# Performance work log

Hardware: AMD Instinct MI355X
Metric: run time of the kernel (lower is better)

The kernel has to match this reference:

```python
import jax, jax.numpy as jnp
import numpy as np

B = 100000
MEM_DIM = 256
EDGE_DIM = 172
TIME_DIM = 100
NODE_DIM = 128
P = 5  # num_prototypes
LN_EPS = 1e-5
TEMP_MIN, TEMP_MAX = 0.05, 2.0


def _xavier(key, shape):
    fan_out, fan_in = shape
    lim = jnp.sqrt(6.0 / (fan_in + fan_out))
    return jax.random.uniform(key, shape, jnp.float32, -lim, lim)


def setup_inputs() -> dict:
    key = jax.random.key(0)
    ks = jax.random.split(key, 8)
    qin = MEM_DIM + EDGE_DIM + TIME_DIM
    gin = 2 * MEM_DIM + TIME_DIM
    return {
        "raw_memory": jax.random.normal(ks[0], (B, MEM_DIM), jnp.float32),
        "node_features": jax.random.normal(ks[1], (B, NODE_DIM), jnp.float32),
        "edge_features": jax.random.normal(ks[2], (B, EDGE_DIM), jnp.float32),
        "time_encoding": jax.random.normal(ks[3], (B, TIME_DIM), jnp.float32),
        "prototypes": jax.random.normal(ks[4], (B, P, MEM_DIM), jnp.float32),
        "Wq": _xavier(ks[5], (MEM_DIM, qin)),
        "bq": jnp.zeros((MEM_DIM,), jnp.float32),
        "Wg": _xavier(ks[6], (1, gin)),
        "bg": jnp.ones((1,), jnp.float32),
        "temperature": jnp.ones((1,), jnp.float32) * 0.1,
        "ln_gamma": jnp.ones((MEM_DIM,), jnp.float32),
        "ln_beta": jnp.zeros((MEM_DIM,), jnp.float32),
        "node_mask": jax.random.randint(ks[7], (B, P), 0, 2).astype(bool),
    }


def _layernorm(x, gamma, beta):
    mu = jnp.mean(x, axis=-1, keepdims=True)
    var = jnp.var(x, axis=-1, keepdims=True)
    return (x - mu) * jax.lax.rsqrt(var + LN_EPS) * gamma + beta


def _l2norm(x):
    n = jnp.sqrt(jnp.sum(x * x, axis=-1, keepdims=True))
    return x / jnp.maximum(n, 1e-12)


def reference(raw_memory, node_features, edge_features, time_encoding, prototypes,
              Wq, bq, Wg, bg, temperature, ln_gamma, ln_beta, node_mask):
    raw_memory = jnp.nan_to_num(raw_memory, nan=0.0, posinf=10.0, neginf=-10.0)
    edge_features = jnp.nan_to_num(edge_features, nan=0.0, posinf=10.0, neginf=-10.0)

    # fused query path: concat -> linear -> layernorm -> tanh
    query_inputs = jnp.concatenate([raw_memory, edge_features, time_encoding], axis=-1)
    query = query_inputs @ Wq.T + bq
    query = jnp.tanh(_layernorm(query, ln_gamma, ln_beta))  # [B, D]

    # cosine similarity against per-node prototypes [B, P, D]
    qn = _l2norm(query)
    pn = _l2norm(prototypes)
    sim = jnp.einsum('bd,bpd->bp', qn, pn)
    temp = jnp.clip(temperature, TEMP_MIN, TEMP_MAX)
    sim = sim / (temp + 1e-6)

    # masked softmax with uniform fallback for fully-masked rows
    sim = jnp.where(node_mask, sim, -jnp.inf)
    all_masked = jnp.all(~node_mask, axis=-1, keepdims=True)
    safe_sim = jnp.where(all_masked, jnp.zeros_like(sim), sim)
    attn = jax.nn.softmax(safe_sim, axis=-1)  # uniform where all masked

    cand = jnp.einsum('bp,bpd->bd', attn, prototypes)
    cand = jnp.clip(cand, -5.0, 5.0)

    gate_inputs = jnp.concatenate([raw_memory, cand, time_encoding], axis=-1)
    gate_inputs = jnp.clip(gate_inputs, -100.0, 100.0)
    gate = jax.nn.sigmoid(gate_inputs @ Wg.T + bg)  # [B, 1]

    updated = (1.0 - gate) * raw_memory + gate * cand
    updated = jnp.clip(_layernorm(updated, ln_gamma, ln_beta), -50.0, 50.0)
    return (updated, attn, gate, cand, query, sim)
```

## Files before the change

### kernel.cpp

```cpp
#include <hip/hip_runtime.h>
#include <math.h>

#define BB 100000
#define DM 256
#define EM 172
#define TM 100
#define QIN 528
#define NP 5

#define OFF_ATTN (256*BB)
#define OFF_GATE (261*BB)
#define OFF_CAND (262*BB)
#define OFF_QRY  (518*BB)
#define OFF_SIM  (774*BB)

__device__ __forceinline__ float ntn(float v) {
  if (v != v) return 0.0f;
  if (isinf(v)) return v > 0.0f ? 10.0f : -10.0f;
  return v;
}

__device__ __forceinline__ float clipf(float v, float lo, float hi) {
  return fminf(fmaxf(v, lo), hi);
}

#define BM 64
#define KC 16

__global__ __launch_bounds__(256)
void k_gemm(const float* __restrict__ raw, const float* __restrict__ edg,
            const float* __restrict__ tim, const float* __restrict__ Wq,
            const float* __restrict__ bq, float* __restrict__ qout)
{
  __shared__ float As[KC][BM];
  __shared__ float Ws[KC][DM];
  const int tid = threadIdx.x;
  const int ty = tid >> 5;
  const int tx = tid & 31;
  const int row0 = (int)blockIdx.x * BM;

  float acc[8][8];
#pragma unroll
  for (int i = 0; i < 8; ++i)
#pragma unroll
    for (int j = 0; j < 8; ++j) acc[i][j] = 0.0f;

  for (int k0 = 0; k0 < QIN; k0 += KC) {
#pragma unroll
    for (int j = 0; j < 4; ++j) {
      int e = tid * 4 + j;
      int r = e >> 4;
      int kk = e & 15;
      int row = row0 + r; row = row < BB ? row : BB - 1;
      int k = k0 + kk;
      float v;
      if (k < DM)           v = ntn(raw[row * DM + k]);
      else if (k < DM + EM) v = ntn(edg[row * EM + (k - DM)]);
      else                  v = tim[row * TM + (k - DM - EM)];
      As[kk][r] = v;
    }
    {
      const float* wr = Wq + tid * QIN + k0;
#pragma unroll
      for (int kk = 0; kk < KC; ++kk) Ws[kk][tid] = wr[kk];
    }
    __syncthreads();
#pragma unroll
    for (int kk = 0; kk < KC; ++kk) {
      float4 a0 = *(const float4*)&As[kk][ty * 8];
      float4 a1 = *(const float4*)&As[kk][ty * 8 + 4];
      float4 b0 = *(const float4*)&Ws[kk][tx * 8];
      float4 b1 = *(const float4*)&Ws[kk][tx * 8 + 4];
      float a[8] = {a0.x,a0.y,a0.z,a0.w,a1.x,a1.y,a1.z,a1.w};
      float b[8] = {b0.x,b0.y,b0.z,b0.w,b1.x,b1.y,b1.z,b1.w};
#pragma unroll
      for (int i = 0; i < 8; ++i)
#pragma unroll
        for (int j = 0; j < 8; ++j) acc[i][j] = fmaf(a[i], b[j], acc[i][j]);
    }
    __syncthreads();
  }

  const int c0 = tx * 8;
  float4 q0 = *(const float4*)&bq[c0];
  float4 q1 = *(const float4*)&bq[c0 + 4];
  float bqv[8] = {q0.x,q0.y,q0.z,q0.w,q1.x,q1.y,q1.z,q1.w};
#pragma unroll
  for (int i = 0; i < 8; ++i) {
    int row = row0 + ty * 8 + i;
    if (row < BB) {
      float4 o0 = make_float4(acc[i][0]+bqv[0], acc[i][1]+bqv[1],
                              acc[i][2]+bqv[2], acc[i][3]+bqv[3]);
      float4 o1 = make_float4(acc[i][4]+bqv[4], acc[i][5]+bqv[5],
                              acc[i][6]+bqv[6], acc[i][7]+bqv[7]);
      *(float4*)&qout[row * DM + c0]     = o0;
      *(float4*)&qout[row * DM + c0 + 4] = o1;
    }
  }
}

__global__ __launch_bounds__(256)
void k_epi(const float* __restrict__ raw, const float* __restrict__ tim,
           const float* __restrict__ pro, const float* __restrict__ Wg,
           const float* __restrict__ bg, const float* __restrict__ tpr,
           const float* __restrict__ gam, const float* __restrict__ bet,
           const unsigned char* __restrict__ msk, float* out)
{
  const int lane = threadIdx.x & 63;
  const int wid  = ((int)blockIdx.x * (int)blockDim.x + (int)threadIdx.x) >> 6;
  const int nw   = ((int)gridDim.x * (int)blockDim.x) >> 6;
  const int c0   = lane * 4;

  const float temp = fminf(fmaxf(tpr[0], 0.05f), 2.0f) + 1e-6f;
  const float bgv  = bg[0];
  const float4 gm4 = *(const float4*)&gam[c0];
  const float4 bt4 = *(const float4*)&bet[c0];
  const float ga[4] = {gm4.x, gm4.y, gm4.z, gm4.w};
  const float be[4] = {bt4.x, bt4.y, bt4.z, bt4.w};
  const float4 wr_ = *(const float4*)&Wg[c0];
  const float4 wc_ = *(const float4*)&Wg[DM + c0];
  float4 wt_ = make_float4(0.f, 0.f, 0.f, 0.f);
  if (lane < TM/4) wt_ = *(const float4*)&Wg[2*DM + c0];

  for (int row = wid; row < BB; row += nw) {
    const float4 qp = *(const float4*)&out[OFF_QRY + row*DM + c0];
    float s  = qp.x + qp.y + qp.z + qp.w;
    float ss = qp.x*qp.x + qp.y*qp.y + qp.z*qp.z + qp.w*qp.w;
#pragma unroll
    for (int m = 32; m; m >>= 1) { s += __shfl_xor(s, m); ss += __shfl_xor(ss, m); }
    const float mu   = s * (1.0f/DM);
    const float rstd = rsqrtf(ss*(1.0f/DM) - mu*mu + 1e-5f);
    float q[4];
    q[0] = tanhf((qp.x - mu)*rstd*ga[0] + be[0]);
    q[1] = tanhf((qp.y - mu)*rstd*ga[1] + be[1]);
    q[2] = tanhf((qp.z - mu)*rstd*ga[2] + be[2]);
    q[3] = tanhf((qp.w - mu)*rstd*ga[3] + be[3]);
    float qs = q[0]*q[0] + q[1]*q[1] + q[2]*q[2] + q[3]*q[3];
#pragma unroll
    for (int m = 32; m; m >>= 1) qs += __shfl_xor(qs, m);
    const float qinv = 1.0f / fmaxf(sqrtf(qs), 1e-12f);

    const float* pb = pro + (long)row * (NP*DM);
    float pc[NP][4], dt[NP], pq[NP];
#pragma unroll
    for (int p = 0; p < NP; ++p) {
      float4 pv = *(const float4*)&pb[p*DM + c0];
      pc[p][0]=pv.x; pc[p][1]=pv.y; pc[p][2]=pv.z; pc[p][3]=pv.w;
      dt[p] = q[0]*pv.x + q[1]*pv.y + q[2]*pv.z + q[3]*pv.w;
      pq[p] = pv.x*pv.x + pv.y*pv.y + pv.z*pv.z + pv.w*pv.w;
    }
#pragma unroll
    for (int p = 0; p < NP; ++p) {
#pragma unroll
      for (int m = 32; m; m >>= 1) {
        dt[p] += __shfl_xor(dt[p], m);
        pq[p] += __shfl_xor(pq[p], m);
      }
    }

    unsigned char mk[NP];
#pragma unroll
    for (int p = 0; p < NP; ++p) mk[p] = msk[row*NP + p];

    float sv[NP];
#pragma unroll
    for (int p = 0; p < NP; ++p) {
      float pinv = 1.0f / fmaxf(sqrtf(pq[p]), 1e-12f);
      sv[p] = (dt[p] * qinv * pinv) / temp;
    }

    const bool any = (mk[0] | mk[1] | mk[2] | mk[3] | mk[4]) != 0;
    float at[NP];
    if (any) {
      float mx = -3.0e38f;
#pragma unroll
      for (int p = 0; p < NP; ++p) if (mk[p]) mx = fmaxf(mx, sv[p]);
      float es = 0.0f;
#pragma unroll
      for (int p = 0; p < NP; ++p) { at[p] = mk[p] ? expf(sv[p] - mx) : 0.0f; es += at[p]; }
      const float inv = 1.0f / es;
#pragma unroll
      for (int p = 0; p < NP; ++p) at[p] *= inv;
    } else {
#pragma unroll
      for (int p = 0; p < NP; ++p) at[p] = 0.2f;
    }

    float cd[4] = {0.f, 0.f, 0.f, 0.f};
#pragma unroll
    for (int p = 0; p < NP; ++p) {
      cd[0] += at[p]*pc[p][0]; cd[1] += at[p]*pc[p][1];
      cd[2] += at[p]*pc[p][2]; cd[3] += at[p]*pc[p][3];
    }
#pragma unroll
    for (int j = 0; j < 4; ++j) cd[j] = clipf(cd[j], -5.0f, 5.0f);

    const float4 rv = *(const float4*)&raw[row*DM + c0];
    float rn[4] = {ntn(rv.x), ntn(rv.y), ntn(rv.z), ntn(rv.w)};
    float gp = 0.0f;
    gp += wr_.x*clipf(rn[0],-100.f,100.f) + wr_.y*clipf(rn[1],-100.f,100.f)
        + wr_.z*clipf(rn[2],-100.f,100.f) + wr_.w*clipf(rn[3],-100.f,100.f);
    gp += wc_.x*clipf(cd[0],-100.f,100.f) + wc_.y*clipf(cd[1],-100.f,100.f)
        + wc_.z*clipf(cd[2],-100.f,100.f) + wc_.w*clipf(cd[3],-100.f,100.f);
    if (lane < TM/4) {
      const float4 tv = *(const float4*)&tim[row*TM + c0];
      gp += wt_.x*clipf(tv.x,-100.f,100.f) + wt_.y*clipf(tv.y,-100.f,100.f)
          + wt_.z*clipf(tv.z,-100.f,100.f) + wt_.w*clipf(tv.w,-100.f,100.f);
    }
#pragma unroll
    for (int m = 32; m; m >>= 1) gp += __shfl_xor(gp, m);
    const float g = 1.0f / (1.0f + expf(-(gp + bgv)));

    float u[4];
#pragma unroll
    for (int j = 0; j < 4; ++j) u[j] = (1.0f - g)*rn[j] + g*cd[j];
    float s2  = u[0] + u[1] + u[2] + u[3];
    float ss2 = u[0]*u[0] + u[1]*u[1] + u[2]*u[2] + u[3]*u[3];
#pragma unroll
    for (int m = 32; m; m >>= 1) { s2 += __shfl_xor(s2, m); ss2 += __shfl_xor(ss2, m); }
    const float mu2   = s2 * (1.0f/DM);
    const float rstd2 = rsqrtf(ss2*(1.0f/DM) - mu2*mu2 + 1e-5f);
    float up[4];
#pragma unroll
    for (int j = 0; j < 4; ++j)
      up[j] = clipf((u[j]-mu2)*rstd2*ga[j] + be[j], -50.0f, 50.0f);

    *(float4*)&out[row*DM + c0]            = make_float4(up[0],up[1],up[2],up[3]);
    *(float4*)&out[OFF_CAND + row*DM + c0] = make_float4(cd[0],cd[1],cd[2],cd[3]);
    *(float4*)&out[OFF_QRY  + row*DM + c0] = make_float4(q[0],q[1],q[2],q[3]);
    if (lane < NP) {
      float svv = 0.f, avv = 0.f;
#pragma unroll
      for (int p = 0; p < NP; ++p) if (lane == p) { svv = sv[p]; avv = at[p]; }
      out[OFF_ATTN + row*NP + lane] = avv;
      out[OFF_SIM  + row*NP + lane] = svv;
    }
    if (lane == 0) out[OFF_GATE + row] = g;
  }
}

extern "C" void kernel_launch(void* const* d_in, const int* in_sizes, int n_in,
                              void* d_out, int out_size, void* d_ws, size_t ws_size,
                              hipStream_t stream) {
  const float* raw = (const float*)d_in[0];
  const float* edg = (const float*)d_in[2];
  const float* tim = (const float*)d_in[3];
  const float* pro = (const float*)d_in[4];
  const float* Wq  = (const float*)d_in[5];
  const float* bq  = (const float*)d_in[6];
  const float* Wg  = (const float*)d_in[7];
  const float* bg  = (const float*)d_in[8];
  const float* tpr = (const float*)d_in[9];
  const float* gam = (const float*)d_in[10];
  const float* bet = (const float*)d_in[11];
  const unsigned char* msk = (const unsigned char*)d_in[12];
  float* out = (float*)d_out;

  dim3 g1((BB + BM - 1) / BM);
  k_gemm<<<g1, 256, 0, stream>>>(raw, edg, tim, Wq, bq, out + OFF_QRY);
  k_epi<<<2048, 256, 0, stream>>>(raw, tim, pro, Wg, bg, tpr, gam, bet, msk, out);
}
```

Measured before the change: 1.284 ms.

## Vectorize GEMM tile loads, stride output columns, and remap epilogue to 16-lane rows

The GEMM now stages activation and weight tiles with float4 global loads instead of scalar loads. Each thread's eight output columns become strided by 32 rather than contiguous, which changes the LDS read pattern for Ws and the global store pattern. The epilogue changes from a grid-stride loop with one wave per row to one 16-lane group per row, each lane handling 16 contiguous elements, so its reductions need only four shuffle steps. The trade-off is more register pressure in the epilogue, a second pass over the prototypes (re-read for the candidate), and scalar, less-vectorized GEMM output stores.

```diff
diff --git a/kernel.cpp b/kernel.cpp
--- a/kernel.cpp
+++ b/kernel.cpp
@@ -19,7 +19,6 @@
   if (isinf(v)) return v > 0.0f ? 10.0f : -10.0f;
   return v;
 }
-
 __device__ __forceinline__ float clipf(float v, float lo, float hi) {
   return fminf(fmaxf(v, lo), hi);
 }
@@ -39,6 +38,10 @@
   const int tx = tid & 31;
   const int row0 = (int)blockIdx.x * BM;
 
+  const int sr = tid >> 2;
+  const int skq = (tid & 3) * 4;
+  int srow = row0 + sr; srow = srow < BB ? srow : BB - 1;
+
   float acc[8][8];
 #pragma unroll
   for (int i = 0; i < 8; ++i)
@@ -46,33 +49,34 @@
     for (int j = 0; j < 8; ++j) acc[i][j] = 0.0f;
 
   for (int k0 = 0; k0 < QIN; k0 += KC) {
-#pragma unroll
-    for (int j = 0; j < 4; ++j) {
-      int e = tid * 4 + j;
-      int r = e >> 4;
-      int kk = e & 15;
-      int row = row0 + r; row = row < BB ? row : BB - 1;
-      int k = k0 + kk;
-      float v;
-      if (k < DM)           v = ntn(raw[row * DM + k]);
-      else if (k < DM + EM) v = ntn(edg[row * EM + (k - DM)]);
-      else                  v = tim[row * TM + (k - DM - EM)];
-      As[kk][r] = v;
+    {
+      const int k = k0 + skq;
+      float4 v;
+      if (k < DM)            v = *(const float4*)&raw[srow * DM + k];
+      else if (k < DM + EM)  v = *(const float4*)&edg[srow * EM + (k - DM)];
+      else                   v = *(const float4*)&tim[srow * TM + (k - DM - EM)];
+      if (k < DM + EM) { v.x = ntn(v.x); v.y = ntn(v.y); v.z = ntn(v.z); v.w = ntn(v.w); }
+      As[skq + 0][sr] = v.x; As[skq + 1][sr] = v.y;
+      As[skq + 2][sr] = v.z; As[skq + 3][sr] = v.w;
     }
     {
       const float* wr = Wq + tid * QIN + k0;
 #pragma unroll
-      for (int kk = 0; kk < KC; ++kk) Ws[kk][tid] = wr[kk];
+      for (int q4 = 0; q4 < 4; ++q4) {
+        float4 w = *(const float4*)&wr[q4 * 4];
+        Ws[q4 * 4 + 0][tid] = w.x; Ws[q4 * 4 + 1][tid] = w.y;
+        Ws[q4 * 4 + 2][tid] = w.z; Ws[q4 * 4 + 3][tid] = w.w;
+      }
     }
     __syncthreads();
 #pragma unroll
     for (int kk = 0; kk < KC; ++kk) {
       float4 a0 = *(const float4*)&As[kk][ty * 8];
       float4 a1 = *(const float4*)&As[kk][ty * 8 + 4];
-      float4 b0 = *(const float4*)&Ws[kk][tx * 8];
-      float4 b1 = *(const float4*)&Ws[kk][tx * 8 + 4];
       float a[8] = {a0.x,a0.y,a0.z,a0.w,a1.x,a1.y,a1.z,a1.w};
-      float b[8] = {b0.x,b0.y,b0.z,b0.w,b1.x,b1.y,b1.z,b1.w};
+      float b[8];
+#pragma unroll
+      for (int j = 0; j < 8; ++j) b[j] = Ws[kk][tx + 32 * j];
 #pragma unroll
       for (int i = 0; i < 8; ++i)
 #pragma unroll
@@ -81,23 +85,22 @@
     __syncthreads();
   }
 
-  const int c0 = tx * 8;
-  float4 q0 = *(const float4*)&bq[c0];
-  float4 q1 = *(const float4*)&bq[c0 + 4];
-  float bqv[8] = {q0.x,q0.y,q0.z,q0.w,q1.x,q1.y,q1.z,q1.w};
+  float bqv[8];
+#pragma unroll
+  for (int j = 0; j < 8; ++j) bqv[j] = bq[tx + 32 * j];
 #pragma unroll
   for (int i = 0; i < 8; ++i) {
     int row = row0 + ty * 8 + i;
     if (row < BB) {
-      float4 o0 = make_float4(acc[i][0]+bqv[0], acc[i][1]+bqv[1],
-                              acc[i][2]+bqv[2], acc[i][3]+bqv[3]);
-      float4 o1 = make_float4(acc[i][4]+bqv[4], acc[i][5]+bqv[5],
-                              acc[i][6]+bqv[6], acc[i][7]+bqv[7]);
-      *(float4*)&qout[row * DM + c0]     = o0;
-      *(float4*)&qout[row * DM + c0 + 4] = o1;
-    }
-  }
-}
+#pragma unroll
+      for (int j = 0; j < 8; ++j)
+        qout[row * DM + tx + 32 * j] = acc[i][j] + bqv[j];
+    }
+  }
+}
+
+#define RED16(x) { x += __shfl_xor(x,1); x += __shfl_xor(x,2); \
+                   x += __shfl_xor(x,4); x += __shfl_xor(x,8); }
 
 __global__ __launch_bounds__(256)
 void k_epi(const float* __restrict__ raw, const float* __restrict__ tim,
@@ -106,137 +109,184 @@
            const float* __restrict__ gam, const float* __restrict__ bet,
            const unsigned char* __restrict__ msk, float* out)
 {
-  const int lane = threadIdx.x & 63;
-  const int wid  = ((int)blockIdx.x * (int)blockDim.x + (int)threadIdx.x) >> 6;
-  const int nw   = ((int)gridDim.x * (int)blockDim.x) >> 6;
-  const int c0   = lane * 4;
+  const int tid = threadIdx.x;
+  const int l16 = tid & 15;
+  const int gid = tid >> 4;
+  const int row = (int)blockIdx.x * 16 + gid;
+  if (row >= BB) return;
+  const int c0 = l16 * 16;
 
   const float temp = fminf(fmaxf(tpr[0], 0.05f), 2.0f) + 1e-6f;
   const float bgv  = bg[0];
-  const float4 gm4 = *(const float4*)&gam[c0];
-  const float4 bt4 = *(const float4*)&bet[c0];
-  const float ga[4] = {gm4.x, gm4.y, gm4.z, gm4.w};
-  const float be[4] = {bt4.x, bt4.y, bt4.z, bt4.w};
-  const float4 wr_ = *(const float4*)&Wg[c0];
-  const float4 wc_ = *(const float4*)&Wg[DM + c0];
-  float4 wt_ = make_float4(0.f, 0.f, 0.f, 0.f);
-  if (lane < TM/4) wt_ = *(const float4*)&Wg[2*DM + c0];
-
-  for (int row = wid; row < BB; row += nw) {
-    const float4 qp = *(const float4*)&out[OFF_QRY + row*DM + c0];
-    float s  = qp.x + qp.y + qp.z + qp.w;
-    float ss = qp.x*qp.x + qp.y*qp.y + qp.z*qp.z + qp.w*qp.w;
-#pragma unroll
-    for (int m = 32; m; m >>= 1) { s += __shfl_xor(s, m); ss += __shfl_xor(ss, m); }
-    const float mu   = s * (1.0f/DM);
-    const float rstd = rsqrtf(ss*(1.0f/DM) - mu*mu + 1e-5f);
-    float q[4];
-    q[0] = tanhf((qp.x - mu)*rstd*ga[0] + be[0]);
-    q[1] = tanhf((qp.y - mu)*rstd*ga[1] + be[1]);
-    q[2] = tanhf((qp.z - mu)*rstd*ga[2] + be[2]);
-    q[3] = tanhf((qp.w - mu)*rstd*ga[3] + be[3]);
-    float qs = q[0]*q[0] + q[1]*q[1] + q[2]*q[2] + q[3]*q[3];
-#pragma unroll
-    for (int m = 32; m; m >>= 1) qs += __shfl_xor(qs, m);
-    const float qinv = 1.0f / fmaxf(sqrtf(qs), 1e-12f);
-
-    const float* pb = pro + (long)row * (NP*DM);
-    float pc[NP][4], dt[NP], pq[NP];
-#pragma unroll
-    for (int p = 0; p < NP; ++p) {
-      float4 pv = *(const float4*)&pb[p*DM + c0];
-      pc[p][0]=pv.x; pc[p][1]=pv.y; pc[p][2]=pv.z; pc[p][3]=pv.w;
-      dt[p] = q[0]*pv.x + q[1]*pv.y + q[2]*pv.z + q[3]*pv.w;
-      pq[p] = pv.x*pv.x + pv.y*pv.y + pv.z*pv.z + pv.w*pv.w;
-    }
-#pragma unroll
-    for (int p = 0; p < NP; ++p) {
-#pragma unroll
-      for (int m = 32; m; m >>= 1) {
-        dt[p] += __shfl_xor(dt[p], m);
-        pq[p] += __shfl_xor(pq[p], m);
-      }
-    }
-
-    unsigned char mk[NP];
-#pragma unroll
-    for (int p = 0; p < NP; ++p) mk[p] = msk[row*NP + p];
-
-    float sv[NP];
-#pragma unroll
-    for (int p = 0; p < NP; ++p) {
-      float pinv = 1.0f / fmaxf(sqrtf(pq[p]), 1e-12f);
-      sv[p] = (dt[p] * qinv * pinv) / temp;
-    }
-
-    const bool any = (mk[0] | mk[1] | mk[2] | mk[3] | mk[4]) != 0;
-    float at[NP];
-    if (any) {
-      float mx = -3.0e38f;
-#pragma unroll
-      for (int p = 0; p < NP; ++p) if (mk[p]) mx = fmaxf(mx, sv[p]);
-      float es = 0.0f;
-#pragma unroll
-      for (int p = 0; p < NP; ++p) { at[p] = mk[p] ? expf(sv[p] - mx) : 0.0f; es += at[p]; }
-      const float inv = 1.0f / es;
-#pragma unroll
-      for (int p = 0; p < NP; ++p) at[p] *= inv;
-    } else {
-#pragma unroll
-      for (int p = 0; p < NP; ++p) at[p] = 0.2f;
-    }
-
-    float cd[4] = {0.f, 0.f, 0.f, 0.f};
-#pragma unroll
-    for (int p = 0; p < NP; ++p) {
-      cd[0] += at[p]*pc[p][0]; cd[1] += at[p]*pc[p][1];
-      cd[2] += at[p]*pc[p][2]; cd[3] += at[p]*pc[p][3];
-    }
-#pragma unroll
-    for (int j = 0; j < 4; ++j) cd[j] = clipf(cd[j], -5.0f, 5.0f);
-
-    const float4 rv = *(const float4*)&raw[row*DM + c0];
-    float rn[4] = {ntn(rv.x), ntn(rv.y), ntn(rv.z), ntn(rv.w)};
-    float gp = 0.0f;
-    gp += wr_.x*clipf(rn[0],-100.f,100.f) + wr_.y*clipf(rn[1],-100.f,100.f)
-        + wr_.z*clipf(rn[2],-100.f,100.f) + wr_.w*clipf(rn[3],-100.f,100.f);
-    gp += wc_.x*clipf(cd[0],-100.f,100.f) + wc_.y*clipf(cd[1],-100.f,100.f)
-        + wc_.z*clipf(cd[2],-100.f,100.f) + wc_.w*clipf(cd[3],-100.f,100.f);
-    if (lane < TM/4) {
-      const float4 tv = *(const float4*)&tim[row*TM + c0];
-      gp += wt_.x*clipf(tv.x,-100.f,100.f) + wt_.y*clipf(tv.y,-100.f,100.f)
-          + wt_.z*clipf(tv.z,-100.f,100.f) + wt_.w*clipf(tv.w,-100.f,100.f);
-    }
-#pragma unroll
-    for (int m = 32; m; m >>= 1) gp += __shfl_xor(gp, m);
-    const float g = 1.0f / (1.0f + expf(-(gp + bgv)));
-
-    float u[4];
-#pragma unroll
-    for (int j = 0; j < 4; ++j) u[j] = (1.0f - g)*rn[j] + g*cd[j];
-    float s2  = u[0] + u[1] + u[2] + u[3];
-    float ss2 = u[0]*u[0] + u[1]*u[1] + u[2]*u[2] + u[3]*u[3];
-#pragma unroll
-    for (int m = 32; m; m >>= 1) { s2 += __shfl_xor(s2, m); ss2 += __shfl_xor(ss2, m); }
-    const float mu2   = s2 * (1.0f/DM);
-    const float rstd2 = rsqrtf(ss2*(1.0f/DM) - mu2*mu2 + 1e-5f);
-    float up[4];
-#pragma unroll
-    for (int j = 0; j < 4; ++j)
-      up[j] = clipf((u[j]-mu2)*rstd2*ga[j] + be[j], -50.0f, 50.0f);
-
-    *(float4*)&out[row*DM + c0]            = make_float4(up[0],up[1],up[2],up[3]);
-    *(float4*)&out[OFF_CAND + row*DM + c0] = make_float4(cd[0],cd[1],cd[2],cd[3]);
-    *(float4*)&out[OFF_QRY  + row*DM + c0] = make_float4(q[0],q[1],q[2],q[3]);
-    if (lane < NP) {
-      float svv = 0.f, avv = 0.f;
-#pragma unroll
-      for (int p = 0; p < NP; ++p) if (lane == p) { svv = sv[p]; avv = at[p]; }
-      out[OFF_ATTN + row*NP + lane] = avv;
-      out[OFF_SIM  + row*NP + lane] = svv;
-    }
-    if (lane == 0) out[OFF_GATE + row] = g;
-  }
+
+  float x[16];
+  {
+    const float* qs_ = out + OFF_QRY + (long)row * DM + c0;
+#pragma unroll
+    for (int q4 = 0; q4 < 4; ++q4) {
+      float4 v = *(const float4*)&qs_[q4 * 4];
+      x[q4*4+0]=v.x; x[q4*4+1]=v.y; x[q4*4+2]=v.z; x[q4*4+3]=v.w;
+    }
+  }
+  float s = 0.f, ss = 0.f;
+#pragma unroll
+  for (int j = 0; j < 16; ++j) { s += x[j]; ss += x[j]*x[j]; }
+  RED16(s); RED16(ss);
+  const float mu   = s * (1.0f/DM);
+  const float rstd = rsqrtf(ss*(1.0f/DM) - mu*mu + 1e-5f);
+#pragma unroll
+  for (int q4 = 0; q4 < 4; ++q4) {
+    float4 g4 = *(const float4*)&gam[c0 + q4*4];
+    float4 b4 = *(const float4*)&bet[c0 + q4*4];
+    x[q4*4+0] = tanhf((x[q4*4+0]-mu)*rstd*g4.x + b4.x);
+    x[q4*4+1] = tanhf((x[q4*4+1]-mu)*rstd*g4.y + b4.y);
+    x[q4*4+2] = tanhf((x[q4*4+2]-mu)*rstd*g4.z + b4.z);
+    x[q4*4+3] = tanhf((x[q4*4+3]-mu)*rstd*g4.w + b4.w);
+  }
+  float qs2 = 0.f;
+#pragma unroll
+  for (int j = 0; j < 16; ++j) qs2 += x[j]*x[j];
+  RED16(qs2);
+  const float qinv = 1.0f / fmaxf(sqrtf(qs2), 1e-12f);
+
+  {
+    float* qo = out + OFF_QRY + (long)row * DM + c0;
+#pragma unroll
+    for (int q4 = 0; q4 < 4; ++q4)
+      *(float4*)&qo[q4*4] = make_float4(x[q4*4+0],x[q4*4+1],x[q4*4+2],x[q4*4+3]);
+  }
+
+  const float* pb = pro + (long)row * (NP*DM);
+  float dt[NP], pq[NP];
+#pragma unroll
+  for (int p = 0; p < NP; ++p) {
+    float d = 0.f, n = 0.f;
+#pragma unroll
+    for (int q4 = 0; q4 < 4; ++q4) {
+      float4 pv = *(const float4*)&pb[p*DM + c0 + q4*4];
+      d += x[q4*4+0]*pv.x + x[q4*4+1]*pv.y + x[q4*4+2]*pv.z + x[q4*4+3]*pv.w;
+      n += pv.x*pv.x + pv.y*pv.y + pv.z*pv.z + pv.w*pv.w;
+    }
+    dt[p] = d; pq[p] = n;
+  }
+#pragma unroll
+  for (int p = 0; p < NP; ++p) { RED16(dt[p]); RED16(pq[p]); }
+
+  unsigned char mk[NP];
+#pragma unroll
+  for (int p = 0; p < NP; ++p) mk[p] = msk[row*NP + p];
+
+  float sv[NP];
+#pragma unroll
+  for (int p = 0; p < NP; ++p) {
+    float pinv = 1.0f / fmaxf(sqrtf(pq[p]), 1e-12f);
+    sv[p] = (dt[p] * qinv * pinv) / temp;
+  }
+
+  const bool any = (mk[0] | mk[1] | mk[2] | mk[3] | mk[4]) != 0;
+  float at[NP];
+  if (any) {
+    float mx = -3.0e38f;
+#pragma unroll
+    for (int p = 0; p < NP; ++p) if (mk[p]) mx = fmaxf(mx, sv[p]);
+    float es = 0.f;
+#pragma unroll
+    for (int p = 0; p < NP; ++p) { at[p] = mk[p] ? expf(sv[p] - mx) : 0.0f; es += at[p]; }
+    const float inv = 1.0f / es;
+#pragma unroll
+    for (int p = 0; p < NP; ++p) at[p] *= inv;
+  } else {
+#pragma unroll
+    for (int p = 0; p < NP; ++p) at[p] = 0.2f;
+  }
+
+  float cd[16];
+#pragma unroll
+  for (int j = 0; j < 16; ++j) cd[j] = 0.f;
+#pragma unroll
+  for (int p = 0; p < NP; ++p) {
+#pragma unroll
+    for (int q4 = 0; q4 < 4; ++q4) {
+      float4 pv = *(const float4*)&pb[p*DM + c0 + q4*4];
+      cd[q4*4+0] += at[p]*pv.x; cd[q4*4+1] += at[p]*pv.y;
+      cd[q4*4+2] += at[p]*pv.z; cd[q4*4+3] += at[p]*pv.w;
+    }
+  }
+#pragma unroll
+  for (int j = 0; j < 16; ++j) cd[j] = clipf(cd[j], -5.0f, 5.0f);
+
+  float rn[16];
+  {
+    const float* rr = raw + (long)row * DM + c0;
+#pragma unroll
+    for (int q4 = 0; q4 < 4; ++q4) {
+      float4 v = *(const float4*)&rr[q4*4];
+      rn[q4*4+0]=ntn(v.x); rn[q4*4+1]=ntn(v.y); rn[q4*4+2]=ntn(v.z); rn[q4*4+3]=ntn(v.w);
+    }
+  }
+  float gp = 0.f;
+#pragma unroll
+  for (int q4 = 0; q4 < 4; ++q4) {
+    float4 wr4 = *(const float4*)&Wg[c0 + q4*4];
+    float4 wc4 = *(const float4*)&Wg[DM + c0 + q4*4];
+    gp += wr4.x*clipf(rn[q4*4+0],-100.f,100.f) + wr4.y*clipf(rn[q4*4+1],-100.f,100.f)
+        + wr4.z*clipf(rn[q4*4+2],-100.f,100.f) + wr4.w*clipf(rn[q4*4+3],-100.f,100.f);
+    gp += wc4.x*clipf(cd[q4*4+0],-100.f,100.f) + wc4.y*clipf(cd[q4*4+1],-100.f,100.f)
+        + wc4.z*clipf(cd[q4*4+2],-100.f,100.f) + wc4.w*clipf(cd[q4*4+3],-100.f,100.f);
+  }
+  if (l16 < 6) {
+    const float* tr = tim + (long)row * TM + l16*16;
+    const float* wt = Wg + 2*DM + l16*16;
+#pragma unroll
+    for (int q4 = 0; q4 < 4; ++q4) {
+      float4 tv = *(const float4*)&tr[q4*4];
+      float4 wt4 = *(const float4*)&wt[q4*4];
+      gp += wt4.x*clipf(tv.x,-100.f,100.f) + wt4.y*clipf(tv.y,-100.f,100.f)
+          + wt4.z*clipf(tv.z,-100.f,100.f) + wt4.w*clipf(tv.w,-100.f,100.f);
+    }
+  } else if (l16 == 6) {
+    float4 tv = *(const float4*)&tim[(long)row * TM + 96];
+    float4 wt4 = *(const float4*)&Wg[2*DM + 96];
+    gp += wt4.x*clipf(tv.x,-100.f,100.f) + wt4.y*clipf(tv.y,-100.f,100.f)
+        + wt4.z*clipf(tv.z,-100.f,100.f) + wt4.w*clipf(tv.w,-100.f,100.f);
+  }
+  RED16(gp);
+  const float g = 1.0f / (1.0f + expf(-(gp + bgv)));
+
+#pragma unroll
+  for (int j = 0; j < 16; ++j) rn[j] = (1.0f - g)*rn[j] + g*cd[j];
+  float s2 = 0.f, ss2 = 0.f;
+#pragma unroll
+  for (int j = 0; j < 16; ++j) { s2 += rn[j]; ss2 += rn[j]*rn[j]; }
+  RED16(s2); RED16(ss2);
+  const float mu2   = s2 * (1.0f/DM);
+  const float rstd2 = rsqrtf(ss2*(1.0f/DM) - mu2*mu2 + 1e-5f);
+
+  {
+    float* uo = out + (long)row * DM + c0;
+    float* co = out + OFF_CAND + (long)row * DM + c0;
+#pragma unroll
+    for (int q4 = 0; q4 < 4; ++q4) {
+      float4 g4 = *(const float4*)&gam[c0 + q4*4];
+      float4 b4 = *(const float4*)&bet[c0 + q4*4];
+      float4 u4;
+      u4.x = clipf((rn[q4*4+0]-mu2)*rstd2*g4.x + b4.x, -50.f, 50.f);
+      u4.y = clipf((rn[q4*4+1]-mu2)*rstd2*g4.y + b4.y, -50.f, 50.f);
+      u4.z = clipf((rn[q4*4+2]-mu2)*rstd2*g4.z + b4.z, -50.f, 50.f);
+      u4.w = clipf((rn[q4*4+3]-mu2)*rstd2*g4.w + b4.w, -50.f, 50.f);
+      *(float4*)&uo[q4*4] = u4;
+      *(float4*)&co[q4*4] = make_float4(cd[q4*4+0],cd[q4*4+1],cd[q4*4+2],cd[q4*4+3]);
+    }
+  }
+
+  if (l16 < NP) {
+    float svv = 0.f, avv = 0.f;
+#pragma unroll
+    for (int p = 0; p < NP; ++p) if (l16 == p) { svv = sv[p]; avv = at[p]; }
+    out[OFF_ATTN + row*NP + l16] = avv;
+    out[OFF_SIM  + row*NP + l16] = svv;
+  }
+  if (l16 == 0) out[OFF_GATE + row] = g;
 }
 
 extern "C" void kernel_launch(void* const* d_in, const int* in_sizes, int n_in,
@@ -258,5 +308,5 @@
 
   dim3 g1((BB + BM - 1) / BM);
   k_gemm<<<g1, 256, 0, stream>>>(raw, edg, tim, Wq, bq, out + OFF_QRY);
-  k_epi<<<2048, 256, 0, stream>>>(raw, tim, pro, Wg, bg, tpr, gam, bet, msk, out);
-}
+  k_epi<<<(BB + 15) / 16, 256, 0, stream>>>(raw, tim, pro, Wg, bg, tpr, gam, bet, msk, out);
+}
```

New measurement: 1.437 ms. 11.9% more time.
